# Kernel optimization log

Measured on AMD Instinct MI355X. Metric: run time of the kernel, lower is better.

## Reference

```python
import jax, jax.numpy as jnp
import numpy as np

IN_DIM, HID = 256, 10
B, H, W = 4, 128, 128
ADJ = np.array([
    [0,1,0,0,0,0],
    [1,0,1,1,1,1],
    [0,1,0,0,0,0],
    [0,1,0,0,0,0],
    [0,1,0,0,0,1],
    [0,1,0,0,1,0]], dtype=np.int32)
EDGES = np.argwhere(ADJ)                      # [E,2] rows = (src, dst), torch.nonzero order
SRC = jnp.asarray(EDGES[:, 0])
DST = jnp.asarray(EDGES[:, 1])
HALF_IDX = jnp.asarray([0, 0, 0, 0, 1, 1])    # parts 1-4 -> upper half, 5-6 -> lower half


def _grouped_att(x, Wg, bg):
    # grouped 1x1 conv (groups=n, one output channel per node) + sigmoid
    # x [n,B,h,H,W], Wg [n,h], bg [n] -> [n,B,1,H,W]
    return jax.nn.sigmoid(jnp.einsum('nbchw,nc->nbhw', x, Wg) + bg[:, None, None, None])[:, :, None]


def _composition(x, Wg, bg):
    # attention-gated sum of child node states -> message [B,h,H,W]
    return (_grouped_att(x, Wg, bg) * x).sum(0)


def _part_dependency(fea, x, Wf, Wx, b):
    # relu(conv1x1(cat([fea, x_i], ch))) per node; fea contribution computed once
    # fea [B,C,H,W], x [n,B,h,H,W] -> [n,B,h,H,W]
    f = jnp.einsum('bchw,oc->bohw', fea, Wf)
    return jax.nn.relu(f[None] + jnp.einsum('nbchw,oc->nbohw', x, Wx)
                       + b[None, None, :, None, None])


def _decomposition(fea, x_src, x_dst, Wf, Wx, b):
    # att = sigmoid(conv1x1(cat([fea, x_dst]))) with per-node weights; gates x_src
    att = jax.nn.sigmoid(jnp.einsum('bchw,nc->nbhw', fea, Wf)
                         + jnp.einsum('nbchw,nc->nbhw', x_dst, Wx)
                         + b[:, None, None, None])[:, :, None]
    return att * x_src


def _att_update(x, m, Wa, ba, Wu):
    # attention-gated fused update; x,m [n,B,h,H,W]; Wa [n,1,2h], Wu [n,h,2h]
    cat = jnp.concatenate([x, m], axis=2)
    att = jax.nn.sigmoid(jnp.einsum('nbchw,noc->nbohw', cat, Wa) + ba[:, None, :, None, None])
    upd = jax.nn.relu(jnp.einsum('nbchw,noc->nbohw', cat, Wu))
    return x * (1.0 - att) + upd * att


def _gnn(P):
    xp, xh, xf, p_fea, h_fea = P['xp'], P['xh'], P['xf'], P['p_fea'], P['h_fea']
    # ---------- Full graph ----------
    xf_msg = _composition(xh, P['Wf_comp'], P['bf_comp'])
    xf_new = _att_update(xf[None], xf_msg[None], P['Wf_uatt'], P['bf_uatt'], P['Wf_uupd'])
    # ---------- Half graph ----------
    h_dp = _part_dependency(h_fea, xh, P['Wh_pdp_f'], P['Wh_pdp_x'], P['bh_pdp'])  # [2,B,h,H,W]
    h_att = _grouped_att(xh, P['Wh_att'], P['bh_att'])                              # [2,B,1,H,W]
    xphu = _composition(xp[:4], P['Wh_cu'], P['bh_cu'])
    xphl = _composition(xp[4:], P['Wh_cl'], P['bh_cl'])
    xlh = h_dp[1] * h_att[1] * (1.0 - h_att[0])   # lower -> upper
    xuh = h_dp[0] * h_att[0] * (1.0 - h_att[1])   # upper -> lower
    xfh = _decomposition(h_fea, xf[None], xh, P['Wh_dec_f'], P['Wh_dec_x'], P['bh_dec'])
    h_msg = jnp.stack([xphu + xlh, xphl + xuh]) + xfh
    xh_new = _att_update(xh, h_msg, P['Wh_uatt'], P['bh_uatt'], P['Wh_uupd'])
    # ---------- Part graph: edge-wise gather + segment-sum scatter ----------
    p_dp = _part_dependency(p_fea, xp, P['Wp_pdp_f'], P['Wp_pdp_x'], P['bp_pdp'])  # [6,B,h,H,W]
    p_att = _grouped_att(xp, P['Wp_att'], P['bp_att'])                              # [6,B,1,H,W]
    e_msg = p_dp[SRC] * p_att[SRC] * (1.0 - p_att[DST])                             # [E,B,h,H,W]
    xpp = jax.ops.segment_sum(e_msg, DST, num_segments=6)
    xhp = _decomposition(p_fea, xh[HALF_IDX], xp, P['Wp_dec_f'], P['Wp_dec_x'], P['bp_dec'])
    xp_new = _att_update(xp, xpp + xhp, P['Wp_uatt'], P['bp_uatt'], P['Wp_uupd'])
    # stacked node states: 6 parts, 2 halves, 1 full -> [9,B,h,H,W]
    return jnp.concatenate([xp_new, xh_new, xf_new], axis=0)


def setup_inputs() -> dict:
    key = jax.random.key(0)
    ks = iter(jax.random.split(key, 64))
    def rnd(shape, s=1.0):
        return jax.random.normal(next(ks), shape, dtype=jnp.float32) * s
    return {
        'xp': rnd((6, B, HID, H, W)),
        'xh': rnd((2, B, HID, H, W)),
        'xf': rnd((B, HID, H, W)),
        'bg_node': rnd((B, HID, H, W)),
        'p_fea': rnd((B, IN_DIM, H, W)),
        'h_fea': rnd((B, IN_DIM, H, W)),
        'f_fea': rnd((B, IN_DIM, H, W)),
        'Wf_comp': rnd((2, HID), 0.3), 'bf_comp': rnd((2,), 0.1),
        'Wf_uatt': rnd((1, 1, 2 * HID), 0.3), 'bf_uatt': rnd((1, 1), 0.1),
        'Wf_uupd': rnd((1, HID, 2 * HID), 0.3),
        'Wh_pdp_f': rnd((HID, IN_DIM), 0.05), 'Wh_pdp_x': rnd((HID, HID), 0.3), 'bh_pdp': rnd((HID,), 0.1),
        'Wh_att': rnd((2, HID), 0.3), 'bh_att': rnd((2,), 0.1),
        'Wh_cu': rnd((4, HID), 0.3), 'bh_cu': rnd((4,), 0.1),
        'Wh_cl': rnd((2, HID), 0.3), 'bh_cl': rnd((2,), 0.1),
        'Wh_dec_f': rnd((2, IN_DIM), 0.05), 'Wh_dec_x': rnd((2, HID), 0.3), 'bh_dec': rnd((2,), 0.1),
        'Wh_uatt': rnd((2, 1, 2 * HID), 0.3), 'bh_uatt': rnd((2, 1), 0.1),
        'Wh_uupd': rnd((2, HID, 2 * HID), 0.3),
        'Wp_pdp_f': rnd((HID, IN_DIM), 0.05), 'Wp_pdp_x': rnd((HID, HID), 0.3), 'bp_pdp': rnd((HID,), 0.1),
        'Wp_att': rnd((6, HID), 0.3), 'bp_att': rnd((6,), 0.1),
        'Wp_dec_f': rnd((6, IN_DIM), 0.05), 'Wp_dec_x': rnd((6, HID), 0.3), 'bp_dec': rnd((6,), 0.1),
        'Wp_uatt': rnd((6, 1, 2 * HID), 0.3), 'bp_uatt': rnd((6, 1), 0.1),
        'Wp_uupd': rnd((6, HID, 2 * HID), 0.3),
    }


def reference(xp, xh, xf, bg_node, p_fea, h_fea, f_fea,
              Wf_comp, bf_comp, Wf_uatt, bf_uatt, Wf_uupd,
              Wh_pdp_f, Wh_pdp_x, bh_pdp, Wh_att, bh_att,
              Wh_cu, bh_cu, Wh_cl, bh_cl,
              Wh_dec_f, Wh_dec_x, bh_dec, Wh_uatt, bh_uatt, Wh_uupd,
              Wp_pdp_f, Wp_pdp_x, bp_pdp, Wp_att, bp_att,
              Wp_dec_f, Wp_dec_x, bp_dec, Wp_uatt, bp_uatt, Wp_uupd):
    P = dict(locals())
    return _gnn(P)
```

## Files before the change

### kernel.cpp

```cpp
#include <hip/hip_runtime.h>


namespace {
constexpr int S     = 128 * 128;
constexpr int BATCH = 4;
constexpr int HID   = 10;
constexpr int INDIM = 256;
constexpr int NPIX  = BATCH * S;

struct Ptrs {
  const float* __restrict__ xp;
  const float* __restrict__ xh;
  const float* __restrict__ xf;
  const float* __restrict__ p_fea;
  const float* __restrict__ h_fea;
  const float* __restrict__ Wf_comp;  const float* __restrict__ bf_comp;
  const float* __restrict__ Wf_uatt;  const float* __restrict__ bf_uatt;
  const float* __restrict__ Wf_uupd;
  const float* __restrict__ Wh_pdp_f; const float* __restrict__ Wh_pdp_x;
  const float* __restrict__ bh_pdp;
  const float* __restrict__ Wh_att;   const float* __restrict__ bh_att;
  const float* __restrict__ Wh_cu;    const float* __restrict__ bh_cu;
  const float* __restrict__ Wh_cl;    const float* __restrict__ bh_cl;
  const float* __restrict__ Wh_dec_f; const float* __restrict__ Wh_dec_x;
  const float* __restrict__ bh_dec;
  const float* __restrict__ Wh_uatt;  const float* __restrict__ bh_uatt;
  const float* __restrict__ Wh_uupd;
  const float* __restrict__ Wp_pdp_f; const float* __restrict__ Wp_pdp_x;
  const float* __restrict__ bp_pdp;
  const float* __restrict__ Wp_att;   const float* __restrict__ bp_att;
  const float* __restrict__ Wp_dec_f; const float* __restrict__ Wp_dec_x;
  const float* __restrict__ bp_dec;
  const float* __restrict__ Wp_uatt;  const float* __restrict__ bp_uatt;
  const float* __restrict__ Wp_uupd;
  float* __restrict__ out;
  float* __restrict__ ws;
};

__device__ __forceinline__ float sigmoidf(float x) {
  return 1.0f / (1.0f + __expf(-x));
}


constexpr int LROW = 33;

template <int NO>
__device__ __forceinline__ void proj_impl(
    float* lds,
    const float* __restrict__ fea,
    const float* __restrict__ Wa,
    const float* __restrict__ Wb,
    float* __restrict__ ws, int obase) {
  const int t   = threadIdx.x;
  const int pxg = t & 63;
  const int sl  = __builtin_amdgcn_readfirstlane(t >> 6);
  const int pb  = blockIdx.x * 128;
  const int b   = pb >> 14;
  const int p0  = pb & (S - 1);

  float2 acc[NO];
#pragma unroll
  for (int o = 0; o < NO; ++o) { acc[o].x = 0.f; acc[o].y = 0.f; }

  const float2* __restrict__ base =
      (const float2*)fea + (((size_t)(b * INDIM + sl * 64) * S + p0) >> 1) + pxg;
#pragma unroll
  for (int cl = 0; cl < 64; ++cl) {
    const int c = sl * 64 + cl;
    const float2 v = base[(size_t)cl * (S / 2)];
#pragma unroll
    for (int o = 0; o < 10; ++o) {
      const float w = Wa[o * INDIM + c];
      acc[o].x = fmaf(v.x, w, acc[o].x);
      acc[o].y = fmaf(v.y, w, acc[o].y);
    }
#pragma unroll
    for (int o = 10; o < NO; ++o) {
      const float w = Wb[(o - 10) * INDIM + c];
      acc[o].x = fmaf(v.x, w, acc[o].x);
      acc[o].y = fmaf(v.y, w, acc[o].y);
    }
  }

  float* row = lds + (sl * 64 + pxg) * LROW;
#pragma unroll
  for (int o = 0; o < NO; ++o) {
    row[2 * o]     = acc[o].x;
    row[2 * o + 1] = acc[o].y;
  }
  __syncthreads();

  constexpr int K = NO / 4;
  const int og = t >> 6;
#pragma unroll
  for (int k = 0; k < K; ++k) {
    const int o = og * K + k;
    float sx = 0.f, sy = 0.f;
#pragma unroll
    for (int s2 = 0; s2 < 4; ++s2) {
      const float* r2 = lds + (s2 * 64 + pxg) * LROW;
      sx += r2[2 * o];
      sy += r2[2 * o + 1];
    }
    float2 res; res.x = sx; res.y = sy;
    *(float2*)(ws + (size_t)(obase + o) * NPIX + pb + pxg * 2) = res;
  }
}

__global__ __launch_bounds__(256) void proj_kernel(Ptrs P) {
  __shared__ float lds[4 * 64 * LROW];
  if (blockIdx.y == 0) {
    proj_impl<12>(lds, P.h_fea, P.Wh_pdp_f, P.Wh_dec_f, P.ws, 0);
  } else {
    proj_impl<16>(lds, P.p_fea, P.Wp_pdp_f, P.Wp_dec_f, P.ws, 12);
  }
}


__device__ __forceinline__ void att_update_store(
    const float* x, const float* m,
    const float* __restrict__ Wa, float ba, const float* __restrict__ Wu,
    float* __restrict__ outp) {
  float a = ba;
#pragma unroll
  for (int c = 0; c < HID; ++c) a = fmaf(x[c], Wa[c], a);
#pragma unroll
  for (int c = 0; c < HID; ++c) a = fmaf(m[c], Wa[HID + c], a);
  a = sigmoidf(a);
#pragma unroll
  for (int o = 0; o < HID; ++o) {
    float u = 0.f;
#pragma unroll
    for (int c = 0; c < HID; ++c) u = fmaf(x[c], Wu[o * 2 * HID + c], u);
#pragma unroll
    for (int c = 0; c < HID; ++c) u = fmaf(m[c], Wu[o * 2 * HID + HID + c], u);
    u = fmaxf(u, 0.f);
    outp[(size_t)o * S] = x[o] * (1.f - a) + u * a;
  }
}

__global__ __launch_bounds__(256) void gnn_main(Ptrs P) {
  const int tid = blockIdx.x * blockDim.x + threadIdx.x;
  const int b = tid >> 14;
  const int p = tid & (S - 1);

  float fh[HID], fpj[HID], pdec[6];
#pragma unroll
  for (int o = 0; o < HID; ++o) fh[o] = P.ws[(size_t)o * NPIX + tid];
  const float hdec0 = P.ws[(size_t)10 * NPIX + tid];
  const float hdec1 = P.ws[(size_t)11 * NPIX + tid];
#pragma unroll
  for (int o = 0; o < HID; ++o) fpj[o] = P.ws[(size_t)(12 + o) * NPIX + tid];
#pragma unroll
  for (int n = 0; n < 6; ++n) pdec[n] = P.ws[(size_t)(22 + n) * NPIX + tid];

  float xh0[HID], xh1[HID], xfv[HID];
#pragma unroll
  for (int c = 0; c < HID; ++c) {
    xh0[c] = P.xh[((size_t)(0 * BATCH + b) * HID + c) * S + p];
    xh1[c] = P.xh[((size_t)(1 * BATCH + b) * HID + c) * S + p];
    xfv[c] = P.xf[((size_t)b * HID + c) * S + p];
  }
  float xp[6][HID];
#pragma unroll
  for (int n = 0; n < 6; ++n)
#pragma unroll
    for (int c = 0; c < HID; ++c)
      xp[n][c] = P.xp[((size_t)(n * BATCH + b) * HID + c) * S + p];

  {
    float a0 = P.bf_comp[0], a1 = P.bf_comp[1];
#pragma unroll
    for (int c = 0; c < HID; ++c) {
      a0 = fmaf(xh0[c], P.Wf_comp[c], a0);
      a1 = fmaf(xh1[c], P.Wf_comp[HID + c], a1);
    }
    a0 = sigmoidf(a0); a1 = sigmoidf(a1);
    float msg[HID];
#pragma unroll
    for (int c = 0; c < HID; ++c) msg[c] = a0 * xh0[c] + a1 * xh1[c];
    att_update_store(xfv, msg, P.Wf_uatt, P.bf_uatt[0], P.Wf_uupd,
                     P.out + ((size_t)(8 * BATCH + b) * HID) * S + p);
  }

  {
    float hatt0 = P.bh_att[0], hatt1 = P.bh_att[1];
#pragma unroll
    for (int c = 0; c < HID; ++c) {
      hatt0 = fmaf(xh0[c], P.Wh_att[c], hatt0);
      hatt1 = fmaf(xh1[c], P.Wh_att[HID + c], hatt1);
    }
    hatt0 = sigmoidf(hatt0); hatt1 = sigmoidf(hatt1);

    float xphu[HID] = {}, xphl[HID] = {};
#pragma unroll
    for (int i = 0; i < 4; ++i) {
      float s = P.bh_cu[i];
#pragma unroll
      for (int c = 0; c < HID; ++c) s = fmaf(xp[i][c], P.Wh_cu[i * HID + c], s);
      s = sigmoidf(s);
#pragma unroll
      for (int c = 0; c < HID; ++c) xphu[c] = fmaf(s, xp[i][c], xphu[c]);
    }
#pragma unroll
    for (int i = 0; i < 2; ++i) {
      float s = P.bh_cl[i];
#pragma unroll
      for (int c = 0; c < HID; ++c) s = fmaf(xp[4 + i][c], P.Wh_cl[i * HID + c], s);
      s = sigmoidf(s);
#pragma unroll
      for (int c = 0; c < HID; ++c) xphl[c] = fmaf(s, xp[4 + i][c], xphl[c]);
    }

    float d0 = hdec0 + P.bh_dec[0], d1 = hdec1 + P.bh_dec[1];
#pragma unroll
    for (int c = 0; c < HID; ++c) {
      d0 = fmaf(xh0[c], P.Wh_dec_x[c], d0);
      d1 = fmaf(xh1[c], P.Wh_dec_x[HID + c], d1);
    }
    d0 = sigmoidf(d0); d1 = sigmoidf(d1);

    const float wl = hatt1 * (1.f - hatt0);
    const float wu = hatt0 * (1.f - hatt1);

    float m0[HID], m1[HID];
#pragma unroll
    for (int o = 0; o < HID; ++o) {
      const float base_o = fh[o] + P.bh_pdp[o];
      float dp0 = base_o, dp1 = base_o;
#pragma unroll
      for (int c = 0; c < HID; ++c) {
        dp0 = fmaf(xh0[c], P.Wh_pdp_x[o * HID + c], dp0);
        dp1 = fmaf(xh1[c], P.Wh_pdp_x[o * HID + c], dp1);
      }
      dp0 = fmaxf(dp0, 0.f);
      dp1 = fmaxf(dp1, 0.f);
      m0[o] = xphu[o] + dp1 * wl + d0 * xfv[o];
      m1[o] = xphl[o] + dp0 * wu + d1 * xfv[o];
    }
    att_update_store(xh0, m0, P.Wh_uatt + 0 * 2 * HID, P.bh_uatt[0],
                     P.Wh_uupd + 0 * HID * 2 * HID,
                     P.out + ((size_t)(6 * BATCH + b) * HID) * S + p);
    att_update_store(xh1, m1, P.Wh_uatt + 1 * 2 * HID, P.bh_uatt[1],
                     P.Wh_uupd + 1 * HID * 2 * HID,
                     P.out + ((size_t)(7 * BATCH + b) * HID) * S + p);
  }

  {
    float patt[6];
#pragma unroll
    for (int n = 0; n < 6; ++n) {
      float s = P.bp_att[n];
#pragma unroll
      for (int c = 0; c < HID; ++c) s = fmaf(xp[n][c], P.Wp_att[n * HID + c], s);
      patt[n] = sigmoidf(s);
    }

    float g1[HID], gOth[HID] = {}, g4[HID], g5[HID];
#pragma unroll
    for (int n = 0; n < 6; ++n) {
#pragma unroll
      for (int o = 0; o < HID; ++o) {
        float dp = fpj[o] + P.bp_pdp[o];
#pragma unroll
        for (int c = 0; c < HID; ++c) dp = fmaf(xp[n][c], P.Wp_pdp_x[o * HID + c], dp);
        dp = fmaxf(dp, 0.f) * patt[n];
        if (n == 1) g1[o] = dp; else gOth[o] += dp;
        if (n == 4) g4[o] = dp;
        if (n == 5) g5[o] = dp;
      }
    }

#pragma unroll
    for (int n = 0; n < 6; ++n) {
      const float onem = 1.f - patt[n];
      float dg = pdec[n] + P.bp_dec[n];
#pragma unroll
      for (int c = 0; c < HID; ++c) dg = fmaf(xp[n][c], P.Wp_dec_x[n * HID + c], dg);
      dg = sigmoidf(dg);

      float m[HID];
#pragma unroll
      for (int o = 0; o < HID; ++o) {
        float sum;
        if (n == 0 || n == 2 || n == 3) sum = g1[o];
        else if (n == 1)                sum = gOth[o];
        else if (n == 4)                sum = g1[o] + g5[o];
        else                            sum = g1[o] + g4[o];
        const float xh_src = (n < 4) ? xh0[o] : xh1[o];
        m[o] = onem * sum + dg * xh_src;
      }
      att_update_store(xp[n], m, P.Wp_uatt + n * 2 * HID, P.bp_uatt[n],
                       P.Wp_uupd + n * HID * 2 * HID,
                       P.out + ((size_t)(n * BATCH + b) * HID) * S + p);
    }
  }
}

}

extern "C" void kernel_launch(void* const* d_in, const int* in_sizes, int n_in,
                              void* d_out, int out_size, void* d_ws, size_t ws_size,
                              hipStream_t stream) {
  Ptrs P;
  P.xp       = (const float*)d_in[0];
  P.xh       = (const float*)d_in[1];
  P.xf       = (const float*)d_in[2];
  P.p_fea    = (const float*)d_in[4];
  P.h_fea    = (const float*)d_in[5];
  P.Wf_comp  = (const float*)d_in[7];
  P.bf_comp  = (const float*)d_in[8];
  P.Wf_uatt  = (const float*)d_in[9];
  P.bf_uatt  = (const float*)d_in[10];
  P.Wf_uupd  = (const float*)d_in[11];
  P.Wh_pdp_f = (const float*)d_in[12];
  P.Wh_pdp_x = (const float*)d_in[13];
  P.bh_pdp   = (const float*)d_in[14];
  P.Wh_att   = (const float*)d_in[15];
  P.bh_att   = (const float*)d_in[16];
  P.Wh_cu    = (const float*)d_in[17];
  P.bh_cu    = (const float*)d_in[18];
  P.Wh_cl    = (const float*)d_in[19];
  P.bh_cl    = (const float*)d_in[20];
  P.Wh_dec_f = (const float*)d_in[21];
  P.Wh_dec_x = (const float*)d_in[22];
  P.bh_dec   = (const float*)d_in[23];
  P.Wh_uatt  = (const float*)d_in[24];
  P.bh_uatt  = (const float*)d_in[25];
  P.Wh_uupd  = (const float*)d_in[26];
  P.Wp_pdp_f = (const float*)d_in[27];
  P.Wp_pdp_x = (const float*)d_in[28];
  P.bp_pdp   = (const float*)d_in[29];
  P.Wp_att   = (const float*)d_in[30];
  P.bp_att   = (const float*)d_in[31];
  P.Wp_dec_f = (const float*)d_in[32];
  P.Wp_dec_x = (const float*)d_in[33];
  P.bp_dec   = (const float*)d_in[34];
  P.Wp_uatt  = (const float*)d_in[35];
  P.bp_uatt  = (const float*)d_in[36];
  P.Wp_uupd  = (const float*)d_in[37];
  P.out      = (float*)d_out;
  P.ws       = (float*)d_ws;

  proj_kernel<<<dim3(NPIX / 128, 2), dim3(256), 0, stream>>>(P);
  gnn_main<<<dim3(NPIX / 256), dim3(256), 0, stream>>>(P);
}
```

Before: 76.82 us.

## Split GNN update across per-node grid dimension and widen projection to float4

The main GNN kernel is split so that each of 9 blockIdx.y slices computes one output node (6 parts, 2 halves, full), instead of one thread doing every node. Each slice reloads only the inputs it needs and recomputes the shared part-dependency terms for its neighbour sources. This cuts per-thread register pressure and raises parallelism, at the cost of redundant loads and recomputation. The projection kernel now processes 4 pixels per thread with float4 loads, software-prefetches 8 channels ahead, uses a wider LDS row stride and launch bounds of 2 blocks.

Measured after the change: 70.72 us. -7.9%, faster.

```diff
diff --git a/kernel.cpp b/kernel.cpp
--- a/kernel.cpp
+++ b/kernel.cpp
@@ -42,7 +42,7 @@
 }
 
 
-constexpr int LROW = 33;
+constexpr int LROW = 65;
 
 template <int NO>
 __device__ __forceinline__ void proj_impl(
@@ -54,39 +54,63 @@
   const int t   = threadIdx.x;
   const int pxg = t & 63;
   const int sl  = __builtin_amdgcn_readfirstlane(t >> 6);
-  const int pb  = blockIdx.x * 128;
+  const int pb  = blockIdx.x * 256;
   const int b   = pb >> 14;
   const int p0  = pb & (S - 1);
 
-  float2 acc[NO];
-#pragma unroll
-  for (int o = 0; o < NO; ++o) { acc[o].x = 0.f; acc[o].y = 0.f; }
-
-  const float2* __restrict__ base =
-      (const float2*)fea + (((size_t)(b * INDIM + sl * 64) * S + p0) >> 1) + pxg;
-#pragma unroll
-  for (int cl = 0; cl < 64; ++cl) {
-    const int c = sl * 64 + cl;
-    const float2 v = base[(size_t)cl * (S / 2)];
-#pragma unroll
-    for (int o = 0; o < 10; ++o) {
-      const float w = Wa[o * INDIM + c];
-      acc[o].x = fmaf(v.x, w, acc[o].x);
-      acc[o].y = fmaf(v.y, w, acc[o].y);
-    }
-#pragma unroll
-    for (int o = 10; o < NO; ++o) {
-      const float w = Wb[(o - 10) * INDIM + c];
-      acc[o].x = fmaf(v.x, w, acc[o].x);
-      acc[o].y = fmaf(v.y, w, acc[o].y);
+  float4 acc[NO];
+#pragma unroll
+  for (int o = 0; o < NO; ++o) acc[o] = float4{0.f, 0.f, 0.f, 0.f};
+
+  const float4* __restrict__ base =
+      (const float4*)(fea + (size_t)(b * INDIM + sl * 64) * S + p0) + pxg;
+
+  float4 cur[8];
+#pragma unroll
+  for (int i = 0; i < 8; ++i) cur[i] = base[(size_t)i * (S / 4)];
+
+#pragma unroll
+  for (int blk = 0; blk < 8; ++blk) {
+    float4 nxt[8];
+    if (blk < 7) {
+#pragma unroll
+      for (int i = 0; i < 8; ++i)
+        nxt[i] = base[(size_t)((blk + 1) * 8 + i) * (S / 4)];
+    }
+#pragma unroll
+    for (int i = 0; i < 8; ++i) {
+      const int c = sl * 64 + blk * 8 + i;
+      const float4 v = cur[i];
+#pragma unroll
+      for (int o = 0; o < 10; ++o) {
+        const float w = Wa[o * INDIM + c];
+        acc[o].x = fmaf(v.x, w, acc[o].x);
+        acc[o].y = fmaf(v.y, w, acc[o].y);
+        acc[o].z = fmaf(v.z, w, acc[o].z);
+        acc[o].w = fmaf(v.w, w, acc[o].w);
+      }
+#pragma unroll
+      for (int o = 10; o < NO; ++o) {
+        const float w = Wb[(o - 10) * INDIM + c];
+        acc[o].x = fmaf(v.x, w, acc[o].x);
+        acc[o].y = fmaf(v.y, w, acc[o].y);
+        acc[o].z = fmaf(v.z, w, acc[o].z);
+        acc[o].w = fmaf(v.w, w, acc[o].w);
+      }
+    }
+    if (blk < 7) {
+#pragma unroll
+      for (int i = 0; i < 8; ++i) cur[i] = nxt[i];
     }
   }
 
   float* row = lds + (sl * 64 + pxg) * LROW;
 #pragma unroll
   for (int o = 0; o < NO; ++o) {
-    row[2 * o]     = acc[o].x;
-    row[2 * o + 1] = acc[o].y;
+    row[4 * o + 0] = acc[o].x;
+    row[4 * o + 1] = acc[o].y;
+    row[4 * o + 2] = acc[o].z;
+    row[4 * o + 3] = acc[o].w;
   }
   __syncthreads();
 
@@ -95,20 +119,20 @@
 #pragma unroll
   for (int k = 0; k < K; ++k) {
     const int o = og * K + k;
-    float sx = 0.f, sy = 0.f;
+    float r[4] = {0.f, 0.f, 0.f, 0.f};
 #pragma unroll
     for (int s2 = 0; s2 < 4; ++s2) {
-      const float* r2 = lds + (s2 * 64 + pxg) * LROW;
-      sx += r2[2 * o];
-      sy += r2[2 * o + 1];
-    }
-    float2 res; res.x = sx; res.y = sy;
-    *(float2*)(ws + (size_t)(obase + o) * NPIX + pb + pxg * 2) = res;
-  }
-}
-
-__global__ __launch_bounds__(256) void proj_kernel(Ptrs P) {
-  __shared__ float lds[4 * 64 * LROW];
+      const float* rr = lds + (s2 * 64 + pxg) * LROW + 4 * o;
+#pragma unroll
+      for (int j = 0; j < 4; ++j) r[j] += rr[j];
+    }
+    float4 res; res.x = r[0]; res.y = r[1]; res.z = r[2]; res.w = r[3];
+    *(float4*)(ws + (size_t)(obase + o) * NPIX + pb + pxg * 4) = res;
+  }
+}
+
+__global__ __launch_bounds__(256, 2) void proj_kernel(Ptrs P) {
+  __shared__ float lds[256 * LROW];
   if (blockIdx.y == 0) {
     proj_impl<12>(lds, P.h_fea, P.Wh_pdp_f, P.Wh_dec_f, P.ws, 0);
   } else {
@@ -139,36 +163,24 @@
   }
 }
 
-__global__ __launch_bounds__(256) void gnn_main(Ptrs P) {
+__device__ __forceinline__ void load10(float* dst, const float* __restrict__ src,
+                                       int plane, int p) {
+#pragma unroll
+  for (int c = 0; c < HID; ++c)
+    dst[c] = src[((size_t)plane * HID + c) * S + p];
+}
+
+__global__ __launch_bounds__(256) void gnn_node(Ptrs P) {
   const int tid = blockIdx.x * blockDim.x + threadIdx.x;
   const int b = tid >> 14;
   const int p = tid & (S - 1);
-
-  float fh[HID], fpj[HID], pdec[6];
-#pragma unroll
-  for (int o = 0; o < HID; ++o) fh[o] = P.ws[(size_t)o * NPIX + tid];
-  const float hdec0 = P.ws[(size_t)10 * NPIX + tid];
-  const float hdec1 = P.ws[(size_t)11 * NPIX + tid];
-#pragma unroll
-  for (int o = 0; o < HID; ++o) fpj[o] = P.ws[(size_t)(12 + o) * NPIX + tid];
-#pragma unroll
-  for (int n = 0; n < 6; ++n) pdec[n] = P.ws[(size_t)(22 + n) * NPIX + tid];
-
-  float xh0[HID], xh1[HID], xfv[HID];
-#pragma unroll
-  for (int c = 0; c < HID; ++c) {
-    xh0[c] = P.xh[((size_t)(0 * BATCH + b) * HID + c) * S + p];
-    xh1[c] = P.xh[((size_t)(1 * BATCH + b) * HID + c) * S + p];
-    xfv[c] = P.xf[((size_t)b * HID + c) * S + p];
-  }
-  float xp[6][HID];
-#pragma unroll
-  for (int n = 0; n < 6; ++n)
-#pragma unroll
-    for (int c = 0; c < HID; ++c)
-      xp[n][c] = P.xp[((size_t)(n * BATCH + b) * HID + c) * S + p];
-
-  {
+  const int y = blockIdx.y;
+
+  if (y == 8) {
+    float xh0[HID], xh1[HID], xfv[HID];
+    load10(xh0, P.xh, 0 * BATCH + b, p);
+    load10(xh1, P.xh, 1 * BATCH + b, p);
+    load10(xfv, P.xf, b, p);
     float a0 = P.bf_comp[0], a1 = P.bf_comp[1];
 #pragma unroll
     for (int c = 0; c < HID; ++c) {
@@ -181,119 +193,116 @@
     for (int c = 0; c < HID; ++c) msg[c] = a0 * xh0[c] + a1 * xh1[c];
     att_update_store(xfv, msg, P.Wf_uatt, P.bf_uatt[0], P.Wf_uupd,
                      P.out + ((size_t)(8 * BATCH + b) * HID) * S + p);
-  }
-
-  {
-    float hatt0 = P.bh_att[0], hatt1 = P.bh_att[1];
+  } else if (y >= 6) {
+    const int h = y - 6;
+    float xh_self[HID], xh_oth[HID], xfv[HID], fh[HID];
+    load10(xh_self, P.xh, h * BATCH + b, p);
+    load10(xh_oth,  P.xh, (1 - h) * BATCH + b, p);
+    load10(xfv, P.xf, b, p);
+#pragma unroll
+    for (int o = 0; o < HID; ++o) fh[o] = P.ws[(size_t)o * NPIX + tid];
+    const float hdec = P.ws[(size_t)(10 + h) * NPIX + tid];
+
+    const int nsrc = h ? 2 : 4;
+    const int sbase = h ? 4 : 0;
+    const float* __restrict__ Wc = h ? P.Wh_cl : P.Wh_cu;
+    const float* __restrict__ bc = h ? P.bh_cl : P.bh_cu;
+    float comp[HID];
+#pragma unroll
+    for (int o = 0; o < HID; ++o) comp[o] = 0.f;
+#pragma unroll
+    for (int i = 0; i < 4; ++i) {
+      if (i < nsrc) {
+        float xpi[HID];
+        load10(xpi, P.xp, (sbase + i) * BATCH + b, p);
+        float s = bc[i];
+#pragma unroll
+        for (int c = 0; c < HID; ++c) s = fmaf(xpi[c], Wc[i * HID + c], s);
+        s = sigmoidf(s);
+#pragma unroll
+        for (int c = 0; c < HID; ++c) comp[c] = fmaf(s, xpi[c], comp[c]);
+      }
+    }
+
+    float a_self = P.bh_att[h], a_oth = P.bh_att[1 - h];
 #pragma unroll
     for (int c = 0; c < HID; ++c) {
-      hatt0 = fmaf(xh0[c], P.Wh_att[c], hatt0);
-      hatt1 = fmaf(xh1[c], P.Wh_att[HID + c], hatt1);
-    }
-    hatt0 = sigmoidf(hatt0); hatt1 = sigmoidf(hatt1);
-
-    float xphu[HID] = {}, xphl[HID] = {};
-#pragma unroll
-    for (int i = 0; i < 4; ++i) {
-      float s = P.bh_cu[i];
-#pragma unroll
-      for (int c = 0; c < HID; ++c) s = fmaf(xp[i][c], P.Wh_cu[i * HID + c], s);
-      s = sigmoidf(s);
-#pragma unroll
-      for (int c = 0; c < HID; ++c) xphu[c] = fmaf(s, xp[i][c], xphu[c]);
-    }
-#pragma unroll
-    for (int i = 0; i < 2; ++i) {
-      float s = P.bh_cl[i];
-#pragma unroll
-      for (int c = 0; c < HID; ++c) s = fmaf(xp[4 + i][c], P.Wh_cl[i * HID + c], s);
-      s = sigmoidf(s);
-#pragma unroll
-      for (int c = 0; c < HID; ++c) xphl[c] = fmaf(s, xp[4 + i][c], xphl[c]);
-    }
-
-    float d0 = hdec0 + P.bh_dec[0], d1 = hdec1 + P.bh_dec[1];
-#pragma unroll
-    for (int c = 0; c < HID; ++c) {
-      d0 = fmaf(xh0[c], P.Wh_dec_x[c], d0);
-      d1 = fmaf(xh1[c], P.Wh_dec_x[HID + c], d1);
-    }
-    d0 = sigmoidf(d0); d1 = sigmoidf(d1);
-
-    const float wl = hatt1 * (1.f - hatt0);
-    const float wu = hatt0 * (1.f - hatt1);
-
-    float m0[HID], m1[HID];
+      a_self = fmaf(xh_self[c], P.Wh_att[h * HID + c], a_self);
+      a_oth  = fmaf(xh_oth[c],  P.Wh_att[(1 - h) * HID + c], a_oth);
+    }
+    a_self = sigmoidf(a_self); a_oth = sigmoidf(a_oth);
+    const float wg = a_oth * (1.f - a_self);
+
+    float d = hdec + P.bh_dec[h];
+#pragma unroll
+    for (int c = 0; c < HID; ++c) d = fmaf(xh_self[c], P.Wh_dec_x[h * HID + c], d);
+    d = sigmoidf(d);
+
+    float m[HID];
 #pragma unroll
     for (int o = 0; o < HID; ++o) {
-      const float base_o = fh[o] + P.bh_pdp[o];
-      float dp0 = base_o, dp1 = base_o;
-#pragma unroll
-      for (int c = 0; c < HID; ++c) {
-        dp0 = fmaf(xh0[c], P.Wh_pdp_x[o * HID + c], dp0);
-        dp1 = fmaf(xh1[c], P.Wh_pdp_x[o * HID + c], dp1);
+      float dp = fh[o] + P.bh_pdp[o];
+#pragma unroll
+      for (int c = 0; c < HID; ++c) dp = fmaf(xh_oth[c], P.Wh_pdp_x[o * HID + c], dp);
+      dp = fmaxf(dp, 0.f);
+      m[o] = comp[o] + dp * wg + d * xfv[o];
+    }
+    att_update_store(xh_self, m, P.Wh_uatt + h * 2 * HID, P.bh_uatt[h],
+                     P.Wh_uupd + h * HID * 2 * HID,
+                     P.out + ((size_t)((6 + h) * BATCH + b) * HID) * S + p);
+  } else {
+    const int n = y;
+    const int half = (n < 4) ? 0 : 1;
+    const unsigned masks[6] = {0x02u, 0x3Du, 0x02u, 0x02u, 0x22u, 0x12u};
+    const unsigned mask = masks[n];
+
+    float xpn[HID], xh_s[HID], fpj[HID];
+    load10(xpn, P.xp, n * BATCH + b, p);
+    load10(xh_s, P.xh, half * BATCH + b, p);
+#pragma unroll
+    for (int o = 0; o < HID; ++o) fpj[o] = P.ws[(size_t)(12 + o) * NPIX + tid];
+    const float pdecn = P.ws[(size_t)(22 + n) * NPIX + tid];
+
+    float pattn = P.bp_att[n];
+#pragma unroll
+    for (int c = 0; c < HID; ++c) pattn = fmaf(xpn[c], P.Wp_att[n * HID + c], pattn);
+    pattn = sigmoidf(pattn);
+
+    float msum[HID];
+#pragma unroll
+    for (int o = 0; o < HID; ++o) msum[o] = 0.f;
+#pragma unroll
+    for (int src = 0; src < 6; ++src) {
+      if (mask & (1u << src)) {
+        float xps[HID];
+        load10(xps, P.xp, src * BATCH + b, p);
+        float ps = P.bp_att[src];
+#pragma unroll
+        for (int c = 0; c < HID; ++c) ps = fmaf(xps[c], P.Wp_att[src * HID + c], ps);
+        ps = sigmoidf(ps);
+#pragma unroll
+        for (int o = 0; o < HID; ++o) {
+          float dp = fpj[o] + P.bp_pdp[o];
+#pragma unroll
+          for (int c = 0; c < HID; ++c) dp = fmaf(xps[c], P.Wp_pdp_x[o * HID + c], dp);
+          msum[o] = fmaf(fmaxf(dp, 0.f), ps, msum[o]);
+        }
       }
-      dp0 = fmaxf(dp0, 0.f);
-      dp1 = fmaxf(dp1, 0.f);
-      m0[o] = xphu[o] + dp1 * wl + d0 * xfv[o];
-      m1[o] = xphl[o] + dp0 * wu + d1 * xfv[o];
-    }
-    att_update_store(xh0, m0, P.Wh_uatt + 0 * 2 * HID, P.bh_uatt[0],
-                     P.Wh_uupd + 0 * HID * 2 * HID,
-                     P.out + ((size_t)(6 * BATCH + b) * HID) * S + p);
-    att_update_store(xh1, m1, P.Wh_uatt + 1 * 2 * HID, P.bh_uatt[1],
-                     P.Wh_uupd + 1 * HID * 2 * HID,
-                     P.out + ((size_t)(7 * BATCH + b) * HID) * S + p);
-  }
-
-  {
-    float patt[6];
-#pragma unroll
-    for (int n = 0; n < 6; ++n) {
-      float s = P.bp_att[n];
-#pragma unroll
-      for (int c = 0; c < HID; ++c) s = fmaf(xp[n][c], P.Wp_att[n * HID + c], s);
-      patt[n] = sigmoidf(s);
-    }
-
-    float g1[HID], gOth[HID] = {}, g4[HID], g5[HID];
-#pragma unroll
-    for (int n = 0; n < 6; ++n) {
-#pragma unroll
-      for (int o = 0; o < HID; ++o) {
-        float dp = fpj[o] + P.bp_pdp[o];
-#pragma unroll
-        for (int c = 0; c < HID; ++c) dp = fmaf(xp[n][c], P.Wp_pdp_x[o * HID + c], dp);
-        dp = fmaxf(dp, 0.f) * patt[n];
-        if (n == 1) g1[o] = dp; else gOth[o] += dp;
-        if (n == 4) g4[o] = dp;
-        if (n == 5) g5[o] = dp;
-      }
-    }
-
-#pragma unroll
-    for (int n = 0; n < 6; ++n) {
-      const float onem = 1.f - patt[n];
-      float dg = pdec[n] + P.bp_dec[n];
-#pragma unroll
-      for (int c = 0; c < HID; ++c) dg = fmaf(xp[n][c], P.Wp_dec_x[n * HID + c], dg);
-      dg = sigmoidf(dg);
-
-      float m[HID];
-#pragma unroll
-      for (int o = 0; o < HID; ++o) {
-        float sum;
-        if (n == 0 || n == 2 || n == 3) sum = g1[o];
-        else if (n == 1)                sum = gOth[o];
-        else if (n == 4)                sum = g1[o] + g5[o];
-        else                            sum = g1[o] + g4[o];
-        const float xh_src = (n < 4) ? xh0[o] : xh1[o];
-        m[o] = onem * sum + dg * xh_src;
-      }
-      att_update_store(xp[n], m, P.Wp_uatt + n * 2 * HID, P.bp_uatt[n],
-                       P.Wp_uupd + n * HID * 2 * HID,
-                       P.out + ((size_t)(n * BATCH + b) * HID) * S + p);
-    }
+    }
+
+    float dg = pdecn + P.bp_dec[n];
+#pragma unroll
+    for (int c = 0; c < HID; ++c) dg = fmaf(xpn[c], P.Wp_dec_x[n * HID + c], dg);
+    dg = sigmoidf(dg);
+
+    const float onem = 1.f - pattn;
+    float m[HID];
+#pragma unroll
+    for (int o = 0; o < HID; ++o) m[o] = onem * msum[o] + dg * xh_s[o];
+
+    att_update_store(xpn, m, P.Wp_uatt + n * 2 * HID, P.bp_uatt[n],
+                     P.Wp_uupd + n * HID * 2 * HID,
+                     P.out + ((size_t)(n * BATCH + b) * HID) * S + p);
   }
 }
 
@@ -342,6 +351,6 @@
   P.out      = (float*)d_out;
   P.ws       = (float*)d_ws;
 
-  proj_kernel<<<dim3(NPIX / 128, 2), dim3(256), 0, stream>>>(P);
-  gnn_main<<<dim3(NPIX / 256), dim3(256), 0, stream>>>(P);
-}
+  proj_kernel<<<dim3(NPIX / 256, 2), dim3(256), 0, stream>>>(P);
+  gnn_node<<<dim3(NPIX / 256, 9), dim3(256), 0, stream>>>(P);
+}
```

## Fuse feature projection into GNN kernel, splitting half and part branches across grid

Applied to the files above, without the earlier changes.

Merges the two launches into one kernel. Each block computes its 1x1 projection of h_fea or p_fea into registers through LDS, with float4 loads and a 16-deep register prefetch ring, then runs either the half/full-graph branch or the part-graph branch. This removes the 28-plane workspace write and reread plus one launch. The cost is that xh and xp are now loaded in both branches, and xp is reloaded several times inside the part branch, trading register pressure for repeated global loads.

After: 69.39 us. 1.11x faster.

```diff
diff --git a/kernel.cpp b/kernel.cpp
--- a/kernel.cpp
+++ b/kernel.cpp
@@ -7,6 +7,9 @@
 constexpr int HID   = 10;
 constexpr int INDIM = 256;
 constexpr int NPIX  = BATCH * S;
+
+constexpr int LROW = 65;
+constexpr int RD   = 16;
 
 struct Ptrs {
   const float* __restrict__ xp;
@@ -34,88 +37,121 @@
   const float* __restrict__ Wp_uatt;  const float* __restrict__ bp_uatt;
   const float* __restrict__ Wp_uupd;
   float* __restrict__ out;
-  float* __restrict__ ws;
 };
 
 __device__ __forceinline__ float sigmoidf(float x) {
   return 1.0f / (1.0f + __expf(-x));
 }
 
-
-constexpr int LROW = 33;
-
 template <int NO>
-__device__ __forceinline__ void proj_impl(
+__device__ __forceinline__ void proj_to_reg(
     float* lds,
     const float* __restrict__ fea,
     const float* __restrict__ Wa,
     const float* __restrict__ Wb,
-    float* __restrict__ ws, int obase) {
+    float* __restrict__ pr) {
   const int t   = threadIdx.x;
   const int pxg = t & 63;
   const int sl  = __builtin_amdgcn_readfirstlane(t >> 6);
-  const int pb  = blockIdx.x * 128;
+  const int pb  = blockIdx.x * 256;
   const int b   = pb >> 14;
   const int p0  = pb & (S - 1);
-
-  float2 acc[NO];
-#pragma unroll
-  for (int o = 0; o < NO; ++o) { acc[o].x = 0.f; acc[o].y = 0.f; }
-
-  const float2* __restrict__ base =
-      (const float2*)fea + (((size_t)(b * INDIM + sl * 64) * S + p0) >> 1) + pxg;
-#pragma unroll
-  for (int cl = 0; cl < 64; ++cl) {
-    const int c = sl * 64 + cl;
-    const float2 v = base[(size_t)cl * (S / 2)];
+  const size_t S4 = S / 4;
+
+  float4 acc[NO];
+#pragma unroll
+  for (int o = 0; o < NO; ++o) acc[o] = float4{0.f, 0.f, 0.f, 0.f};
+
+  const float4* __restrict__ base =
+      (const float4*)(fea + (size_t)(b * INDIM + sl * 64) * S + p0) + pxg;
+
+  float4 ring[RD];
+#pragma unroll
+  for (int i = 0; i < RD; ++i) ring[i] = base[(size_t)i * S4];
+
+#pragma unroll 1
+  for (int cb = 0; cb < 64 - RD; cb += RD) {
+#pragma unroll
+    for (int i = 0; i < RD; ++i) {
+      const float4 v = ring[i];
+      ring[i] = base[(size_t)(cb + RD + i) * S4];
+      const int c = sl * 64 + cb + i;
+#pragma unroll
+      for (int o = 0; o < 10; ++o) {
+        const float w = Wa[o * INDIM + c];
+        acc[o].x = fmaf(v.x, w, acc[o].x);
+        acc[o].y = fmaf(v.y, w, acc[o].y);
+        acc[o].z = fmaf(v.z, w, acc[o].z);
+        acc[o].w = fmaf(v.w, w, acc[o].w);
+      }
+#pragma unroll
+      for (int o = 10; o < NO; ++o) {
+        const float w = Wb[(o - 10) * INDIM + c];
+        acc[o].x = fmaf(v.x, w, acc[o].x);
+        acc[o].y = fmaf(v.y, w, acc[o].y);
+        acc[o].z = fmaf(v.z, w, acc[o].z);
+        acc[o].w = fmaf(v.w, w, acc[o].w);
+      }
+    }
+  }
+#pragma unroll
+  for (int i = 0; i < RD; ++i) {
+    const float4 v = ring[i];
+    const int c = sl * 64 + (64 - RD) + i;
 #pragma unroll
     for (int o = 0; o < 10; ++o) {
       const float w = Wa[o * INDIM + c];
       acc[o].x = fmaf(v.x, w, acc[o].x);
       acc[o].y = fmaf(v.y, w, acc[o].y);
+      acc[o].z = fmaf(v.z, w, acc[o].z);
+      acc[o].w = fmaf(v.w, w, acc[o].w);
     }
 #pragma unroll
     for (int o = 10; o < NO; ++o) {
       const float w = Wb[(o - 10) * INDIM + c];
       acc[o].x = fmaf(v.x, w, acc[o].x);
       acc[o].y = fmaf(v.y, w, acc[o].y);
+      acc[o].z = fmaf(v.z, w, acc[o].z);
+      acc[o].w = fmaf(v.w, w, acc[o].w);
     }
   }
 
   float* row = lds + (sl * 64 + pxg) * LROW;
 #pragma unroll
   for (int o = 0; o < NO; ++o) {
-    row[2 * o]     = acc[o].x;
-    row[2 * o + 1] = acc[o].y;
+    row[4 * o + 0] = acc[o].x;
+    row[4 * o + 1] = acc[o].y;
+    row[4 * o + 2] = acc[o].z;
+    row[4 * o + 3] = acc[o].w;
   }
   __syncthreads();
 
   constexpr int K = NO / 4;
   const int og = t >> 6;
+  float4 res[K];
 #pragma unroll
   for (int k = 0; k < K; ++k) {
     const int o = og * K + k;
-    float sx = 0.f, sy = 0.f;
+    float rr[4] = {0.f, 0.f, 0.f, 0.f};
 #pragma unroll
     for (int s2 = 0; s2 < 4; ++s2) {
-      const float* r2 = lds + (s2 * 64 + pxg) * LROW;
-      sx += r2[2 * o];
-      sy += r2[2 * o + 1];
-    }
-    float2 res; res.x = sx; res.y = sy;
-    *(float2*)(ws + (size_t)(obase + o) * NPIX + pb + pxg * 2) = res;
-  }
-}
-
-__global__ __launch_bounds__(256) void proj_kernel(Ptrs P) {
-  __shared__ float lds[4 * 64 * LROW];
-  if (blockIdx.y == 0) {
-    proj_impl<12>(lds, P.h_fea, P.Wh_pdp_f, P.Wh_dec_f, P.ws, 0);
-  } else {
-    proj_impl<16>(lds, P.p_fea, P.Wp_pdp_f, P.Wp_dec_f, P.ws, 12);
-  }
-}
-
+      const float* rp = lds + (s2 * 64 + pxg) * LROW + 4 * o;
+#pragma unroll
+      for (int j = 0; j < 4; ++j) rr[j] += rp[j];
+    }
+    res[k] = float4{rr[0], rr[1], rr[2], rr[3]};
+  }
+  __syncthreads();
+
+#pragma unroll
+  for (int k = 0; k < K; ++k) {
+    const int o = og * K + k;
+    *(float4*)(lds + o * 256 + pxg * 4) = res[k];
+  }
+  __syncthreads();
+#pragma unroll
+  for (int o = 0; o < NO; ++o) pr[o] = lds[o * 256 + t];
+}
 
 __device__ __forceinline__ void att_update_store(
     const float* x, const float* m,
@@ -139,131 +175,138 @@
   }
 }
 
-__global__ __launch_bounds__(256) void gnn_main(Ptrs P) {
-  const int tid = blockIdx.x * blockDim.x + threadIdx.x;
-  const int b = tid >> 14;
-  const int p = tid & (S - 1);
-
-  float fh[HID], fpj[HID], pdec[6];
-#pragma unroll
-  for (int o = 0; o < HID; ++o) fh[o] = P.ws[(size_t)o * NPIX + tid];
-  const float hdec0 = P.ws[(size_t)10 * NPIX + tid];
-  const float hdec1 = P.ws[(size_t)11 * NPIX + tid];
-#pragma unroll
-  for (int o = 0; o < HID; ++o) fpj[o] = P.ws[(size_t)(12 + o) * NPIX + tid];
-#pragma unroll
-  for (int n = 0; n < 6; ++n) pdec[n] = P.ws[(size_t)(22 + n) * NPIX + tid];
-
-  float xh0[HID], xh1[HID], xfv[HID];
-#pragma unroll
-  for (int c = 0; c < HID; ++c) {
-    xh0[c] = P.xh[((size_t)(0 * BATCH + b) * HID + c) * S + p];
-    xh1[c] = P.xh[((size_t)(1 * BATCH + b) * HID + c) * S + p];
-    xfv[c] = P.xf[((size_t)b * HID + c) * S + p];
-  }
-  float xp[6][HID];
-#pragma unroll
-  for (int n = 0; n < 6; ++n)
-#pragma unroll
-    for (int c = 0; c < HID; ++c)
-      xp[n][c] = P.xp[((size_t)(n * BATCH + b) * HID + c) * S + p];
-
-  {
-    float a0 = P.bf_comp[0], a1 = P.bf_comp[1];
-#pragma unroll
-    for (int c = 0; c < HID; ++c) {
-      a0 = fmaf(xh0[c], P.Wf_comp[c], a0);
-      a1 = fmaf(xh1[c], P.Wf_comp[HID + c], a1);
-    }
-    a0 = sigmoidf(a0); a1 = sigmoidf(a1);
-    float msg[HID];
-#pragma unroll
-    for (int c = 0; c < HID; ++c) msg[c] = a0 * xh0[c] + a1 * xh1[c];
-    att_update_store(xfv, msg, P.Wf_uatt, P.bf_uatt[0], P.Wf_uupd,
-                     P.out + ((size_t)(8 * BATCH + b) * HID) * S + p);
-  }
-
-  {
-    float hatt0 = P.bh_att[0], hatt1 = P.bh_att[1];
-#pragma unroll
-    for (int c = 0; c < HID; ++c) {
-      hatt0 = fmaf(xh0[c], P.Wh_att[c], hatt0);
-      hatt1 = fmaf(xh1[c], P.Wh_att[HID + c], hatt1);
-    }
-    hatt0 = sigmoidf(hatt0); hatt1 = sigmoidf(hatt1);
-
-    float xphu[HID] = {}, xphl[HID] = {};
-#pragma unroll
-    for (int i = 0; i < 4; ++i) {
-      float s = P.bh_cu[i];
-#pragma unroll
-      for (int c = 0; c < HID; ++c) s = fmaf(xp[i][c], P.Wh_cu[i * HID + c], s);
-      s = sigmoidf(s);
-#pragma unroll
-      for (int c = 0; c < HID; ++c) xphu[c] = fmaf(s, xp[i][c], xphu[c]);
-    }
-#pragma unroll
-    for (int i = 0; i < 2; ++i) {
-      float s = P.bh_cl[i];
-#pragma unroll
-      for (int c = 0; c < HID; ++c) s = fmaf(xp[4 + i][c], P.Wh_cl[i * HID + c], s);
-      s = sigmoidf(s);
-#pragma unroll
-      for (int c = 0; c < HID; ++c) xphl[c] = fmaf(s, xp[4 + i][c], xphl[c]);
-    }
-
-    float d0 = hdec0 + P.bh_dec[0], d1 = hdec1 + P.bh_dec[1];
-#pragma unroll
-    for (int c = 0; c < HID; ++c) {
-      d0 = fmaf(xh0[c], P.Wh_dec_x[c], d0);
-      d1 = fmaf(xh1[c], P.Wh_dec_x[HID + c], d1);
-    }
-    d0 = sigmoidf(d0); d1 = sigmoidf(d1);
-
-    const float wl = hatt1 * (1.f - hatt0);
-    const float wu = hatt0 * (1.f - hatt1);
-
-    float m0[HID], m1[HID];
-#pragma unroll
-    for (int o = 0; o < HID; ++o) {
-      const float base_o = fh[o] + P.bh_pdp[o];
-      float dp0 = base_o, dp1 = base_o;
+__device__ __forceinline__ void load10(float* dst, const float* __restrict__ src,
+                                       int plane, int p) {
+#pragma unroll
+  for (int c = 0; c < HID; ++c)
+    dst[c] = src[((size_t)plane * HID + c) * S + p];
+}
+
+__global__ __launch_bounds__(256, 2) void gnn_fused(Ptrs P) {
+  __shared__ float lds[256 * LROW];
+  const int t  = threadIdx.x;
+  const int pb = blockIdx.x * 256;
+  const int b  = pb >> 14;
+  const int p  = (pb & (S - 1)) + t;
+
+  if (blockIdx.y == 0) {
+    float pr[12];
+    proj_to_reg<12>(lds, P.h_fea, P.Wh_pdp_f, P.Wh_dec_f, pr);
+
+    float xh0[HID], xh1[HID], xfv[HID];
+    load10(xh0, P.xh, 0 * BATCH + b, p);
+    load10(xh1, P.xh, 1 * BATCH + b, p);
+    load10(xfv, P.xf, b, p);
+
+    {
+      float a0 = P.bf_comp[0], a1 = P.bf_comp[1];
 #pragma unroll
       for (int c = 0; c < HID; ++c) {
-        dp0 = fmaf(xh0[c], P.Wh_pdp_x[o * HID + c], dp0);
-        dp1 = fmaf(xh1[c], P.Wh_pdp_x[o * HID + c], dp1);
-      }
-      dp0 = fmaxf(dp0, 0.f);
-      dp1 = fmaxf(dp1, 0.f);
-      m0[o] = xphu[o] + dp1 * wl + d0 * xfv[o];
-      m1[o] = xphl[o] + dp0 * wu + d1 * xfv[o];
-    }
-    att_update_store(xh0, m0, P.Wh_uatt + 0 * 2 * HID, P.bh_uatt[0],
-                     P.Wh_uupd + 0 * HID * 2 * HID,
-                     P.out + ((size_t)(6 * BATCH + b) * HID) * S + p);
-    att_update_store(xh1, m1, P.Wh_uatt + 1 * 2 * HID, P.bh_uatt[1],
-                     P.Wh_uupd + 1 * HID * 2 * HID,
-                     P.out + ((size_t)(7 * BATCH + b) * HID) * S + p);
-  }
-
-  {
+        a0 = fmaf(xh0[c], P.Wf_comp[c], a0);
+        a1 = fmaf(xh1[c], P.Wf_comp[HID + c], a1);
+      }
+      a0 = sigmoidf(a0); a1 = sigmoidf(a1);
+      float msg[HID];
+#pragma unroll
+      for (int c = 0; c < HID; ++c) msg[c] = a0 * xh0[c] + a1 * xh1[c];
+      att_update_store(xfv, msg, P.Wf_uatt, P.bf_uatt[0], P.Wf_uupd,
+                       P.out + ((size_t)(8 * BATCH + b) * HID) * S + p);
+    }
+
+    {
+      float hatt0 = P.bh_att[0], hatt1 = P.bh_att[1];
+#pragma unroll
+      for (int c = 0; c < HID; ++c) {
+        hatt0 = fmaf(xh0[c], P.Wh_att[c], hatt0);
+        hatt1 = fmaf(xh1[c], P.Wh_att[HID + c], hatt1);
+      }
+      hatt0 = sigmoidf(hatt0); hatt1 = sigmoidf(hatt1);
+
+      float xphu[HID] = {}, xphl[HID] = {};
+#pragma unroll
+      for (int i = 0; i < 4; ++i) {
+        float xpi[HID];
+        load10(xpi, P.xp, i * BATCH + b, p);
+        float s = P.bh_cu[i];
+#pragma unroll
+        for (int c = 0; c < HID; ++c) s = fmaf(xpi[c], P.Wh_cu[i * HID + c], s);
+        s = sigmoidf(s);
+#pragma unroll
+        for (int c = 0; c < HID; ++c) xphu[c] = fmaf(s, xpi[c], xphu[c]);
+      }
+#pragma unroll
+      for (int i = 0; i < 2; ++i) {
+        float xpi[HID];
+        load10(xpi, P.xp, (4 + i) * BATCH + b, p);
+        float s = P.bh_cl[i];
+#pragma unroll
+        for (int c = 0; c < HID; ++c) s = fmaf(xpi[c], P.Wh_cl[i * HID + c], s);
+        s = sigmoidf(s);
+#pragma unroll
+        for (int c = 0; c < HID; ++c) xphl[c] = fmaf(s, xpi[c], xphl[c]);
+      }
+
+      float d0 = pr[10] + P.bh_dec[0], d1 = pr[11] + P.bh_dec[1];
+#pragma unroll
+      for (int c = 0; c < HID; ++c) {
+        d0 = fmaf(xh0[c], P.Wh_dec_x[c], d0);
+        d1 = fmaf(xh1[c], P.Wh_dec_x[HID + c], d1);
+      }
+      d0 = sigmoidf(d0); d1 = sigmoidf(d1);
+
+      const float wl = hatt1 * (1.f - hatt0);
+      const float wu = hatt0 * (1.f - hatt1);
+
+      float m0[HID], m1[HID];
+#pragma unroll
+      for (int o = 0; o < HID; ++o) {
+        const float base_o = pr[o] + P.bh_pdp[o];
+        float dp0 = base_o, dp1 = base_o;
+#pragma unroll
+        for (int c = 0; c < HID; ++c) {
+          dp0 = fmaf(xh0[c], P.Wh_pdp_x[o * HID + c], dp0);
+          dp1 = fmaf(xh1[c], P.Wh_pdp_x[o * HID + c], dp1);
+        }
+        dp0 = fmaxf(dp0, 0.f);
+        dp1 = fmaxf(dp1, 0.f);
+        m0[o] = xphu[o] + dp1 * wl + d0 * xfv[o];
+        m1[o] = xphl[o] + dp0 * wu + d1 * xfv[o];
+      }
+      att_update_store(xh0, m0, P.Wh_uatt, P.bh_uatt[0], P.Wh_uupd,
+                       P.out + ((size_t)(6 * BATCH + b) * HID) * S + p);
+      att_update_store(xh1, m1, P.Wh_uatt + 2 * HID, P.bh_uatt[1],
+                       P.Wh_uupd + HID * 2 * HID,
+                       P.out + ((size_t)(7 * BATCH + b) * HID) * S + p);
+    }
+  } else {
+    float pr[16];
+    proj_to_reg<16>(lds, P.p_fea, P.Wp_pdp_f, P.Wp_dec_f, pr);
+
+    float xh0[HID], xh1[HID];
+    load10(xh0, P.xh, 0 * BATCH + b, p);
+    load10(xh1, P.xh, 1 * BATCH + b, p);
+
     float patt[6];
 #pragma unroll
     for (int n = 0; n < 6; ++n) {
+      float xpn[HID];
+      load10(xpn, P.xp, n * BATCH + b, p);
       float s = P.bp_att[n];
 #pragma unroll
-      for (int c = 0; c < HID; ++c) s = fmaf(xp[n][c], P.Wp_att[n * HID + c], s);
+      for (int c = 0; c < HID; ++c) s = fmaf(xpn[c], P.Wp_att[n * HID + c], s);
       patt[n] = sigmoidf(s);
     }
 
     float g1[HID], gOth[HID] = {}, g4[HID], g5[HID];
 #pragma unroll
     for (int n = 0; n < 6; ++n) {
+      float xpn[HID];
+      load10(xpn, P.xp, n * BATCH + b, p);
 #pragma unroll
       for (int o = 0; o < HID; ++o) {
-        float dp = fpj[o] + P.bp_pdp[o];
-#pragma unroll
-        for (int c = 0; c < HID; ++c) dp = fmaf(xp[n][c], P.Wp_pdp_x[o * HID + c], dp);
+        float dp = pr[o] + P.bp_pdp[o];
+#pragma unroll
+        for (int c = 0; c < HID; ++c) dp = fmaf(xpn[c], P.Wp_pdp_x[o * HID + c], dp);
         dp = fmaxf(dp, 0.f) * patt[n];
         if (n == 1) g1[o] = dp; else gOth[o] += dp;
         if (n == 4) g4[o] = dp;
@@ -273,10 +316,12 @@
 
 #pragma unroll
     for (int n = 0; n < 6; ++n) {
+      float xpn[HID];
+      load10(xpn, P.xp, n * BATCH + b, p);
       const float onem = 1.f - patt[n];
-      float dg = pdec[n] + P.bp_dec[n];
-#pragma unroll
-      for (int c = 0; c < HID; ++c) dg = fmaf(xp[n][c], P.Wp_dec_x[n * HID + c], dg);
+      float dg = pr[10 + n] + P.bp_dec[n];
+#pragma unroll
+      for (int c = 0; c < HID; ++c) dg = fmaf(xpn[c], P.Wp_dec_x[n * HID + c], dg);
       dg = sigmoidf(dg);
 
       float m[HID];
@@ -290,7 +335,7 @@
         const float xh_src = (n < 4) ? xh0[o] : xh1[o];
         m[o] = onem * sum + dg * xh_src;
       }
-      att_update_store(xp[n], m, P.Wp_uatt + n * 2 * HID, P.bp_uatt[n],
+      att_update_store(xpn, m, P.Wp_uatt + n * 2 * HID, P.bp_uatt[n],
                        P.Wp_uupd + n * HID * 2 * HID,
                        P.out + ((size_t)(n * BATCH + b) * HID) * S + p);
     }
@@ -340,8 +385,6 @@
   P.bp_uatt  = (const float*)d_in[36];
   P.Wp_uupd  = (const float*)d_in[37];
   P.out      = (float*)d_out;
-  P.ws       = (float*)d_ws;
-
-  proj_kernel<<<dim3(NPIX / 128, 2), dim3(256), 0, stream>>>(P);
-  gnn_main<<<dim3(NPIX / 256), dim3(256), 0, stream>>>(P);
-}
+
+  gnn_fused<<<dim3(NPIX / 256, 2), dim3(256), 0, stream>>>(P);
+}
```
